# Performance work log

Hardware: AMD Instinct MI355X
Metric: run time of the kernel (lower is better)

## Reference

```python
import jax, jax.numpy as jnp
import numpy as np

L, B, S, D, H, F = 3, 2, 2048, 256, 8, 1024
DK = D // H
EPS = 1e-7


def _positional_encoding(max_len: int, dim: int) -> jnp.ndarray:
    # pos in [1, max_len], i in [1, dim]; w = pos / 10000**((2*i//2)/dim) == pos / 10000**(i/dim)
    pos = np.arange(1, max_len + 1, dtype=np.float64)[:, None]
    i = np.arange(1, dim + 1)
    w = pos / np.power(10000.0, i.astype(np.float64) / dim)[None, :]
    pe = np.where((i % 2 == 0)[None, :], np.sin(w), np.cos(w))
    return jnp.asarray(pe, jnp.float32)


def _ln(x, g, b):
    mu = jnp.mean(x, axis=-1, keepdims=True)
    var = jnp.mean((x - mu) ** 2, axis=-1, keepdims=True)
    return (x - mu) / jnp.sqrt(var + EPS) * g + b


def setup_inputs() -> dict:
    key = jax.random.key(0)
    ks = jax.random.split(key, 16)
    s = 0.05
    inp = {
        "x": jax.random.normal(ks[0], (B, S, D), jnp.float32),
        "mask": jax.random.randint(ks[1], (B, S, S), 0, 2).astype(bool),
        "pe": _positional_encoding(S, D),
        "Wq": jax.random.normal(ks[2], (L, H, D, DK), jnp.float32) * s,
        "Wk": jax.random.normal(ks[3], (L, H, D, DK), jnp.float32) * s,
        "Wv": jax.random.normal(ks[4], (L, H, D, DK), jnp.float32) * s,
        "Wo": jax.random.normal(ks[5], (L, D, D), jnp.float32) * s,
        "bo": jnp.zeros((L, D), jnp.float32),
        "ln1_g": jnp.ones((L, D), jnp.float32),
        "ln1_b": jnp.zeros((L, D), jnp.float32),
        "W1": jax.random.normal(ks[6], (L, D, F), jnp.float32) * s,
        "b1": jnp.zeros((L, F), jnp.float32),
        "W2": jax.random.normal(ks[7], (L, F, D), jnp.float32) * s,
        "b2": jnp.zeros((L, D), jnp.float32),
        "ln2_g": jnp.ones((L, D), jnp.float32),
        "ln2_b": jnp.zeros((L, D), jnp.float32),
    }
    return inp


def _encoder_layer(x, mask, Wq, Wk, Wv, Wo, bo, ln1_g, ln1_b, W1, b1, W2, b2, ln2_g, ln2_b):
    # all heads batched: [B,S,D] x [H,D,dk] -> [B,H,S,dk]
    q = jnp.einsum('bsd,hdk->bhsk', x, Wq)
    k = jnp.einsum('bsd,hdk->bhsk', x, Wk)
    v = jnp.einsum('bsd,hdk->bhsk', x, Wv)
    scores = jnp.einsum('bhsk,bhtk->bhst', q, k) / jnp.sqrt(jnp.float32(DK))
    neg = -jnp.finfo(jnp.float32).max
    scores = jnp.where(mask[:, None, :, :], neg, scores)
    attn = jax.nn.softmax(scores, axis=-1)
    # concat heads along feature dim (head-major order as torch.cat dim=2)
    o = jnp.einsum('bhst,bhtv->bshv', attn, v).reshape(x.shape[0], x.shape[1], D)
    o = o @ Wo + bo
    x = _ln(o + x, ln1_g, ln1_b)  # post-norm (prenorm=False), dropout_rate=0
    h = jax.nn.relu(x @ W1 + b1) @ W2 + b2
    x = _ln(h + x, ln2_g, ln2_b)
    return x


def reference(x, mask, pe, Wq, Wk, Wv, Wo, bo, ln1_g, ln1_b, W1, b1, W2, b2, ln2_g, ln2_b):
    x = x + pe[None, : x.shape[1], :]
    for l in range(L):
        x = _encoder_layer(x, mask, Wq[l], Wk[l], Wv[l], Wo[l], bo[l], ln1_g[l], ln1_b[l],
                           W1[l], b1[l], W2[l], b2[l], ln2_g[l], ln2_b[l])
    return x
```

## Files before the change

### kernel.cpp

```cpp
#include <hip/hip_runtime.h>
#include <hip/hip_bf16.h>
#include <cfloat>

#define Lc 3
#define Bc 2
#define Sc 2048
#define Dc 256
#define Hc 8
#define DKc 32
#define Fc 1024

typedef __hip_bfloat16 bf16;
typedef short s8v __attribute__((ext_vector_type(8)));
typedef float f4v __attribute__((ext_vector_type(4)));

#define QSCALE 0.25504526036067815f

__device__ __forceinline__ float load_f(const void* p, size_t i, int isbf)
{
    return isbf ? __bfloat162float(((const bf16*)p)[i]) : ((const float*)p)[i];
}

typedef const __attribute__((address_space(1))) char gchar_t;
typedef __attribute__((address_space(3))) char lchar_t;
__device__ __forceinline__ void glds16(const void* g, void* l)
{
    __builtin_amdgcn_global_load_lds((gchar_t*)(size_t)g, (lchar_t*)(size_t)l,
                                     16, 0, 0);
}

#define NBLK_REPACK 2304
#define NBLK_CONV   6942
#define NBLK_PACK   1024
#define NBLK_PE     4096

__global__ __launch_bounds__(256) void prologue_fused(
    const void* __restrict__ x, const void* __restrict__ mask,
    const void* __restrict__ pe,
    const void* Wq, const void* Wk, const void* Wv,
    const void* Wo, const void* W1, const void* W2,
    const void* bo, const void* b1, const void* b2,
    const void* g1, const void* be1, const void* g2, const void* be2,
    bf16* __restrict__ wqkv, bf16* __restrict__ dstb, float* __restrict__ pc,
    unsigned* __restrict__ pmask, float* __restrict__ xf,
    bf16* __restrict__ xb, int* __restrict__ flags)
{
    __shared__ int sf[2];
    int tid = threadIdx.x;
    if (tid < 64) {
        const unsigned short* u16 = (const unsigned short*)x;
        int cnt = 0;
        for (int i = tid; i < 256; i += 64) {
            unsigned e = (u16[2 * i] >> 7) & 0xFF;
            cnt += (e >= 90 && e <= 140) ? 1 : 0;
        }
        #pragma unroll
        for (int d = 1; d < 64; d <<= 1) cnt += __shfl_xor(cnt, d);
        const unsigned* mu = (const unsigned*)mask;
        int c2 = ((mu[tid] & 0xFFFFFF00u) == 0) ? 1 : 0;
        #pragma unroll
        for (int d = 1; d < 64; d <<= 1) c2 += __shfl_xor(c2, d);
        if (tid == 0) {
            sf[0] = (cnt >= 128) ? 1 : 0;
            sf[1] = (c2 >= 48) ? 1 : 0;
            if (blockIdx.x == 0) { flags[0] = sf[0]; flags[1] = sf[1]; }
        }
    }
    __syncthreads();
    int isbf = sf[0], mf = sf[1];
    int blk = blockIdx.x;

    if (blk < NBLK_REPACK) {
        int idx = blk * 256 + tid;
        int l   = idx / (3 * Dc * Dc);
        int rem = idx % (3 * Dc * Dc);
        int col = rem / Dc;
        int d   = rem % Dc;
        int mat = col / Dc;
        int hk  = col % Dc;
        int h = hk / DKc, kk = hk % DKc;
        const void* W = (mat == 0) ? Wq : (mat == 1) ? Wk : Wv;
        float v = load_f(W, (size_t)l * (Hc * Dc * DKc) + h * (Dc * DKc) + d * DKc + kk, isbf);
        wqkv[idx] = __float2bfloat16(v);
    } else if (blk < NBLK_REPACK + NBLK_CONV) {
        const int NB0 = Lc * Dc * Dc;
        const int NB1 = NB0 + Lc * Dc * Fc;
        const int NB2 = NB1 + Lc * Fc * Dc;
        int idx = (blk - NBLK_REPACK) * 256 + tid;
        if (idx < NB2) {
            const void* src; int off;
            if (idx < NB0) {
                int l = idx / (Dc * Dc); int rem = idx % (Dc * Dc);
                int n = rem / Dc, k = rem % Dc;
                src = Wo; off = l * Dc * Dc + k * Dc + n;
            } else if (idx < NB1) {
                int j = idx - NB0;
                int l = j / (Fc * Dc); int rem = j % (Fc * Dc);
                int n = rem / Dc, k = rem % Dc;
                src = W1; off = l * Dc * Fc + k * Fc + n;
            } else {
                int j = idx - NB1;
                int l = j / (Dc * Fc); int rem = j % (Dc * Fc);
                int n = rem / Fc, k = rem % Fc;
                src = W2; off = l * Fc * Dc + k * Dc + n;
            }
            dstb[idx] = __float2bfloat16(load_f(src, off, isbf));
        } else {
            int off = idx - NB2;
            if (off < 7680) {
                const void* src; int lo;
                if (off < 768)       { src = bo;  lo = off; }
                else if (off < 3840) { src = b1;  lo = off - 768; }
                else if (off < 4608) { src = b2;  lo = off - 3840; }
                else if (off < 5376) { src = g1;  lo = off - 4608; }
                else if (off < 6144) { src = be1; lo = off - 5376; }
                else if (off < 6912) { src = g2;  lo = off - 6144; }
                else                 { src = be2; lo = off - 6912; }
                pc[off] = load_f(src, lo, isbf);
            }
        }
    } else if (blk < NBLK_REPACK + NBLK_CONV + NBLK_PACK) {
        int idx = (blk - NBLK_REPACK - NBLK_CONV) * 256 + tid;
        unsigned wb = 0;
        if (mf) {
            const int* mp = (const int*)mask + (size_t)idx * 32;
            #pragma unroll
            for (int u = 0; u < 8; ++u) {
                uint4 q = *(const uint4*)(mp + u * 4);
                wb |= (q.x ? 1u : 0u) << (u * 4);
                wb |= (q.y ? 1u : 0u) << (u * 4 + 1);
                wb |= (q.z ? 1u : 0u) << (u * 4 + 2);
                wb |= (q.w ? 1u : 0u) << (u * 4 + 3);
            }
        } else {
            const unsigned char* mp = (const unsigned char*)mask + (size_t)idx * 32;
            uint4 a = *(const uint4*)mp;
            uint4 bq = *(const uint4*)(mp + 16);
            const unsigned char* ab = (const unsigned char*)&a;
            const unsigned char* bb = (const unsigned char*)&bq;
            #pragma unroll
            for (int j = 0; j < 16; ++j) {
                wb |= (ab[j] ? 1u : 0u) << j;
                wb |= (bb[j] ? 1u : 0u) << (16 + j);
            }
        }
        pmask[idx] = wb;
    } else {
        int idx = (blk - NBLK_REPACK - NBLK_CONV - NBLK_PACK) * 256 + tid;
        int rem = idx % (Sc * Dc);
        float v = load_f(x, idx, isbf) + load_f(pe, rem, isbf);
        xf[idx] = v;
        xb[idx] = __float2bfloat16(v);
    }
}

__global__ __launch_bounds__(256) void gemm_mfma(
    const bf16* __restrict__ A, const bf16* __restrict__ BT,
    const float* __restrict__ bias, void* __restrict__ C,
    int M, int N, int K, int relu, int obf, float ascale, int scale_ncols)
{
    __shared__ __align__(16) short As[4096];
    __shared__ __align__(16) short Bs[4096];
    int tid = threadIdx.x;
    int w = tid >> 6, lane = tid & 63;
    int quad = lane >> 4, l15 = lane & 15;
    int wm0 = (w & 1) * 32, wn0 = (w >> 1) * 32;
    int row0 = blockIdx.y * 64, col0 = blockIdx.x * 64;

    int s0 = w * 128 + lane;
    int s1 = s0 + 64;
    int r0 = s0 >> 3, c0 = ((s0 & 7) ^ (r0 & 7)) * 8;
    int r1 = s1 >> 3, c1 = ((s1 & 7) ^ (r1 & 7)) * 8;
    const bf16* Ag0 = A + (size_t)(row0 + r0) * K + c0;
    const bf16* Ag1 = A + (size_t)(row0 + r1) * K + c1;
    const bf16* Bg0 = BT + (size_t)(col0 + r0) * K + c0;
    const bf16* Bg1 = BT + (size_t)(col0 + r1) * K + c1;
    short* Ad0 = As + w * 1024;
    short* Ad1 = As + w * 1024 + 512;
    short* Bd0 = Bs + w * 1024;
    short* Bd1 = Bs + w * 1024 + 512;

    f4v acc00 = {0.f,0.f,0.f,0.f}, acc01 = acc00, acc10 = acc00, acc11 = acc00;

    int m0 = wm0 + l15, m1 = wm0 + 16 + l15;
    int n0 = wn0 + l15, n1 = wn0 + 16 + l15;
    int sw7 = l15 & 7;

    for (int k0 = 0; k0 < K; k0 += 64) {
        glds16(Ag0 + k0, Ad0);
        glds16(Ag1 + k0, Ad1);
        glds16(Bg0 + k0, Bd0);
        glds16(Bg1 + k0, Bd1);
        __syncthreads();
        #pragma unroll
        for (int kc = 0; kc < 2; ++kc) {
            int sw = ((kc * 4 + quad) ^ sw7) * 8;
            s8v a0 = *(const s8v*)(As + m0 * 64 + sw);
            s8v a1 = *(const s8v*)(As + m1 * 64 + sw);
            s8v b0 = *(const s8v*)(Bs + n0 * 64 + sw);
            s8v b1 = *(const s8v*)(Bs + n1 * 64 + sw);
            acc00 = __builtin_amdgcn_mfma_f32_16x16x32_bf16(a0, b0, acc00, 0, 0, 0);
            acc01 = __builtin_amdgcn_mfma_f32_16x16x32_bf16(a0, b1, acc01, 0, 0, 0);
            acc10 = __builtin_amdgcn_mfma_f32_16x16x32_bf16(a1, b0, acc10, 0, 0, 0);
            acc11 = __builtin_amdgcn_mfma_f32_16x16x32_bf16(a1, b1, acc11, 0, 0, 0);
        }
        __syncthreads();
    }

    float bv0 = bias ? bias[col0 + wn0 + l15] : 0.f;
    float bv1 = bias ? bias[col0 + wn0 + 16 + l15] : 0.f;
    f4v accs[2][2] = {{acc00, acc01}, {acc10, acc11}};
    #pragma unroll
    for (int mt = 0; mt < 2; ++mt) {
        #pragma unroll
        for (int nt = 0; nt < 2; ++nt) {
            int gr = row0 + wm0 + mt * 16 + quad * 4;
            int gc = col0 + wn0 + nt * 16 + l15;
            float badd = nt ? bv1 : bv0;
            float sc = (gc < scale_ncols) ? ascale : 1.f;
            #pragma unroll
            for (int reg = 0; reg < 4; ++reg) {
                float v = accs[mt][nt][reg] * sc + badd;
                if (relu) v = fmaxf(v, 0.f);
                if (obf) ((bf16*)C)[(size_t)(gr + reg) * N + gc] = __float2bfloat16(v);
                else     ((float*)C)[(size_t)(gr + reg) * N + gc] = v;
            }
        }
    }
}

__global__ __launch_bounds__(256) void gemm_mfma32(
    const bf16* __restrict__ A, const bf16* __restrict__ BT,
    const float* __restrict__ bias, void* __restrict__ C,
    int M, int N, int K, int relu, int obf)
{
    __shared__ __align__(16) short As[2048];
    __shared__ __align__(16) short Bs[4096];
    int tid = threadIdx.x;
    int w = tid >> 6, lane = tid & 63;
    int quad = lane >> 4, l15 = lane & 15;
    int wm0 = (w & 1) * 16, wn0 = (w >> 1) * 32;
    int row0 = blockIdx.y * 32, col0 = blockIdx.x * 64;

    int sa = w * 64 + lane;
    int ra = sa >> 3, ca = ((sa & 7) ^ (ra & 7)) * 8;
    int s0 = w * 128 + lane, s1 = s0 + 64;
    int r0 = s0 >> 3, c0 = ((s0 & 7) ^ (r0 & 7)) * 8;
    int r1 = s1 >> 3, c1 = ((s1 & 7) ^ (r1 & 7)) * 8;
    const bf16* Ag  = A + (size_t)(row0 + ra) * K + ca;
    const bf16* Bg0 = BT + (size_t)(col0 + r0) * K + c0;
    const bf16* Bg1 = BT + (size_t)(col0 + r1) * K + c1;
    short* Ad  = As + w * 512;
    short* Bd0 = Bs + w * 1024;
    short* Bd1 = Bs + w * 1024 + 512;

    f4v acc0 = {0.f,0.f,0.f,0.f}, acc1 = acc0;

    int m0 = wm0 + l15;
    int n0 = wn0 + l15, n1 = wn0 + 16 + l15;
    int sw7 = l15 & 7;

    for (int k0 = 0; k0 < K; k0 += 64) {
        glds16(Ag + k0, Ad);
        glds16(Bg0 + k0, Bd0);
        glds16(Bg1 + k0, Bd1);
        __syncthreads();
        #pragma unroll
        for (int kc = 0; kc < 2; ++kc) {
            int sw = ((kc * 4 + quad) ^ sw7) * 8;
            s8v a0 = *(const s8v*)(As + m0 * 64 + sw);
            s8v b0 = *(const s8v*)(Bs + n0 * 64 + sw);
            s8v b1 = *(const s8v*)(Bs + n1 * 64 + sw);
            acc0 = __builtin_amdgcn_mfma_f32_16x16x32_bf16(a0, b0, acc0, 0, 0, 0);
            acc1 = __builtin_amdgcn_mfma_f32_16x16x32_bf16(a0, b1, acc1, 0, 0, 0);
        }
        __syncthreads();
    }

    float bv0 = bias ? bias[col0 + wn0 + l15] : 0.f;
    float bv1 = bias ? bias[col0 + wn0 + 16 + l15] : 0.f;
    f4v accs[2] = {acc0, acc1};
    #pragma unroll
    for (int nt = 0; nt < 2; ++nt) {
        int gr = row0 + wm0 + quad * 4;
        int gc = col0 + wn0 + nt * 16 + l15;
        float badd = nt ? bv1 : bv0;
        #pragma unroll
        for (int reg = 0; reg < 4; ++reg) {
            float v = accs[nt][reg] + badd;
            if (relu) v = fmaxf(v, 0.f);
            if (obf) ((bf16*)C)[(size_t)(gr + reg) * N + gc] = __float2bfloat16(v);
            else     ((float*)C)[(size_t)(gr + reg) * N + gc] = v;
        }
    }
}

__global__ __launch_bounds__(256) void flash_mfma(
    const bf16* __restrict__ qkv, const unsigned* __restrict__ pmask,
    bf16* __restrict__ op0, bf16* __restrict__ op1,
    bf16* __restrict__ op2, bf16* __restrict__ op3,
    float* __restrict__ spart)
{
    __shared__ __align__(16) short Ks[64 * 40];
    __shared__ __align__(16) short Vt[2336];
    __shared__ __align__(16) short Pw[4][16 * 72];

    int tid = threadIdx.x;
    int w = tid >> 6;
    int lane = tid & 63;
    int quad = lane >> 4, l15 = lane & 15;
    int q0 = blockIdx.x * 64;
    int h = blockIdx.y;
    int z = blockIdx.z;
    int b = z >> 2, rng = z & 3;
    bf16* op = (rng == 0) ? op0 : (rng == 1) ? op1 : (rng == 2) ? op2 : op3;

    s8v qfrag = *(const s8v*)(qkv + (size_t)(b * Sc + q0 + w * 16 + l15) * 768 + h * 32 + quad * 8);

    f4v o0 = {0.f,0.f,0.f,0.f}, o1 = o0;
    float ssum[4] = {0.f, 0.f, 0.f, 0.f};

    int st = tid >> 2, sd = (tid & 3) * 8;
    int sig = ((st & 15) << 2) | (st >> 4);
    short* pwv = Pw[w];
    const unsigned* pmrow = pmask + (size_t)b * Sc * (Sc / 32);

    for (int it = 0; it < 8; ++it) {
        int t0 = rng * (Sc / 4) + it * 64;
        __syncthreads();
        {
            const bf16* kvb = qkv + (size_t)(b * Sc + t0 + st) * 768 + h * 32 + sd;
            uint4 kw = *(const uint4*)(kvb + 256);
            *(uint4*)(Ks + st * 40 + sd) = kw;
            uint4 vw = *(const uint4*)(kvb + 512);
            const unsigned short* vu = (const unsigned short*)&vw;
            #pragma unroll
            for (int j = 0; j < 8; ++j) Vt[(sd + j) * 72 + sig + sd] = (short)vu[j];
        }
        unsigned mw0[4], mw1[4];
        #pragma unroll
        for (int reg = 0; reg < 4; ++reg) {
            int row = q0 + w * 16 + quad * 4 + reg;
            const unsigned* pp = pmrow + (size_t)row * (Sc / 32) + (t0 >> 5);
            mw0[reg] = pp[0];
            mw1[reg] = pp[1];
        }
        __syncthreads();

        f4v sfr[4];
        #pragma unroll
        for (int nt = 0; nt < 4; ++nt) {
            s8v kf = *(const s8v*)(Ks + (l15 + 16 * nt) * 40 + quad * 8);
            f4v zz = {0.f,0.f,0.f,0.f};
            sfr[nt] = __builtin_amdgcn_mfma_f32_16x16x32_bf16(qfrag, kf, zz, 0, 0, 0);
        }
        #pragma unroll
        for (int reg = 0; reg < 4; ++reg) {
            unsigned ta = mw0[reg] >> l15;
            unsigned tb = mw1[reg] >> l15;
            float p0 = exp2f(sfr[0][reg]); if (ta & 1u)         p0 = 0.f;
            float p1 = exp2f(sfr[1][reg]); if ((ta >> 16) & 1u) p1 = 0.f;
            float p2 = exp2f(sfr[2][reg]); if (tb & 1u)         p2 = 0.f;
            float p3 = exp2f(sfr[3][reg]); if ((tb >> 16) & 1u) p3 = 0.f;
            ssum[reg] += (p0 + p1) + (p2 + p3);
            __hip_bfloat162 plo = __float22bfloat162_rn(make_float2(p0, p1));
            __hip_bfloat162 phi = __float22bfloat162_rn(make_float2(p2, p3));
            uint2 pk = {*(unsigned*)&plo, *(unsigned*)&phi};
            *(uint2*)(pwv + (quad * 4 + reg) * 72 + l15 * 4) = pk;
        }
        #pragma unroll
        for (int kc = 0; kc < 2; ++kc) {
            s8v pf  = *(const s8v*)(pwv + l15 * 72 + kc * 32 + quad * 8);
            s8v vf0 = *(const s8v*)(Vt + l15 * 72 + kc * 32 + quad * 8 + (l15 & 24));
            s8v vf1 = *(const s8v*)(Vt + (l15 + 16) * 72 + kc * 32 + quad * 8 + ((l15 + 16) & 24));
            o0 = __builtin_amdgcn_mfma_f32_16x16x32_bf16(pf, vf0, o0, 0, 0, 0);
            o1 = __builtin_amdgcn_mfma_f32_16x16x32_bf16(pf, vf1, o1, 0, 0, 0);
        }
    }

    #pragma unroll
    for (int reg = 0; reg < 4; ++reg) {
        #pragma unroll
        for (int d = 1; d < 16; d <<= 1) ssum[reg] += __shfl_xor(ssum[reg], d);
    }

    #pragma unroll
    for (int reg = 0; reg < 4; ++reg) {
        int row = q0 + w * 16 + quad * 4 + reg;
        size_t ob = (size_t)(b * Sc + row) * Dc + h * DKc;
        op[ob + l15]      = __float2bfloat16(o0[reg]);
        op[ob + 16 + l15] = __float2bfloat16(o1[reg]);
        if (l15 == 0)
            spart[((size_t)(rng * Bc + b) * Hc + h) * Sc + row] = ssum[reg];
    }
}

__global__ __launch_bounds__(256) void attn_merge(
    const bf16* __restrict__ op0, const bf16* __restrict__ op1,
    const bf16* __restrict__ op2, const bf16* __restrict__ op3,
    const float* __restrict__ spart, bf16* __restrict__ attn_out)
{
    int t8 = blockIdx.x * 256 + threadIdx.x;
    size_t idx = (size_t)t8 * 8;
    int d = (int)(idx & 255);
    int h = d >> 5;
    int row = (int)((idx >> 8) & (Sc - 1));
    int b = (int)(idx >> 19);
    float s = 0.f;
    #pragma unroll
    for (int r = 0; r < 4; ++r)
        s += spart[((size_t)(r * Bc + b) * Hc + h) * Sc + row];
    float inv = 1.f / fmaxf(s, 1e-30f);

    uint4 a0 = *(const uint4*)(op0 + idx);
    uint4 a1 = *(const uint4*)(op1 + idx);
    uint4 a2 = *(const uint4*)(op2 + idx);
    uint4 a3 = *(const uint4*)(op3 + idx);
    const unsigned short* u0 = (const unsigned short*)&a0;
    const unsigned short* u1 = (const unsigned short*)&a1;
    const unsigned short* u2 = (const unsigned short*)&a2;
    const unsigned short* u3 = (const unsigned short*)&a3;
    unsigned short outv[8];
    #pragma unroll
    for (int j = 0; j < 8; ++j) {
        float o = (__uint_as_float((unsigned)u0[j] << 16) + __uint_as_float((unsigned)u1[j] << 16))
                + (__uint_as_float((unsigned)u2[j] << 16) + __uint_as_float((unsigned)u3[j] << 16));
        bf16 ov = __float2bfloat16(o * inv);
        outv[j] = *(unsigned short*)&ov;
    }
    *(uint4*)(attn_out + idx) = *(uint4*)outv;
}

__global__ __launch_bounds__(256) void add_ln(
    const float* __restrict__ a, float* __restrict__ xf, bf16* __restrict__ xb,
    const float* __restrict__ g, const float* __restrict__ b,
    void* __restrict__ dout, const int* __restrict__ flags)
{
    __shared__ float ws4[2][4];
    int row = blockIdx.x, d = threadIdx.x;
    size_t idx = (size_t)row * Dc + d;
    float v = a[idx] + xf[idx];
    float s = v;
    #pragma unroll
    for (int dd = 1; dd < 64; dd <<= 1) s += __shfl_xor(s, dd);
    if ((d & 63) == 0) ws4[0][d >> 6] = s;
    __syncthreads();
    float mu = (ws4[0][0] + ws4[0][1] + ws4[0][2] + ws4[0][3]) * (1.f / Dc);
    float c = v - mu;
    float q = c * c;
    #pragma unroll
    for (int dd = 1; dd < 64; dd <<= 1) q += __shfl_xor(q, dd);
    if ((d & 63) == 0) ws4[1][d >> 6] = q;
    __syncthreads();
    float var = (ws4[1][0] + ws4[1][1] + ws4[1][2] + ws4[1][3]) * (1.f / Dc);
    float r2 = c * rsqrtf(var + 1e-7f) * g[d] + b[d];
    xf[idx] = r2;
    xb[idx] = __float2bfloat16(r2);
    if (dout) {
        if (flags[0]) ((bf16*)dout)[idx] = __float2bfloat16(r2);
        else          ((float*)dout)[idx] = r2;
    }
}

extern "C" void kernel_launch(void* const* d_in, const int* in_sizes, int n_in,
                              void* d_out, int out_size, void* d_ws, size_t ws_size,
                              hipStream_t stream)
{
    const void* x    = d_in[0];
    const void* mask = d_in[1];
    const void* pe   = d_in[2];
    const void* Wq   = d_in[3];
    const void* Wk   = d_in[4];
    const void* Wv   = d_in[5];
    const void* Wo   = d_in[6];
    const void* bo   = d_in[7];
    const void* ln1g = d_in[8];
    const void* ln1b = d_in[9];
    const void* W1   = d_in[10];
    const void* b1   = d_in[11];
    const void* W2   = d_in[12];
    const void* b2   = d_in[13];
    const void* ln2g = d_in[14];
    const void* ln2b = d_in[15];

    const int M = Bc * Sc;
    char* ws = (char*)d_ws;
    const size_t MB = 1024 * 1024;
    int*      flags    = (int*)ws;
    float*    xf32     = (float*)(ws + 256);
    float*    obuf     = (float*)(ws + 256 + 4 * MB);
    char*     bigc     = ws + 256 + 8 * MB;
    bf16*     xbf      = (bf16*)(ws + 256 + 16 * MB);
    bf16*     attn_out = (bf16*)(ws + 256 + 18 * MB);
    bf16*     wqkv     = (bf16*)(ws + 256 + 20 * MB);
    bf16*     woc      = wqkv + (size_t)Lc * Dc * 3 * Dc;
    bf16*     w1c      = woc + (size_t)Lc * Dc * Dc;
    bf16*     w2c      = w1c + (size_t)Lc * Dc * Fc;
    float*    pc       = (float*)(w2c + (size_t)Lc * Fc * Dc);
    unsigned* pmask    = (unsigned*)(ws + 256 + 25 * MB);
    float*    spart    = (float*)(ws + 256 + 26 * MB);

    bf16* qkv  = (bf16*)bigc;
    bf16* hbuf = (bf16*)bigc;
    bf16* op0  = (bf16*)obuf;
    bf16* op1  = op0 + (size_t)M * Dc;
    bf16* op2  = attn_out;
    bf16* op3  = (bf16*)(bigc + 6 * MB);

    float* pc_bo   = pc;
    float* pc_b1   = pc + 768;
    float* pc_b2   = pc + 3840;
    float* pc_ln1g = pc + 4608;
    float* pc_ln1b = pc + 5376;
    float* pc_ln2g = pc + 6144;
    float* pc_ln2b = pc + 6912;

    prologue_fused<<<NBLK_REPACK + NBLK_CONV + NBLK_PACK + NBLK_PE, 256, 0, stream>>>(
        x, mask, pe, Wq, Wk, Wv, Wo, W1, W2, bo, b1, b2,
        ln1g, ln1b, ln2g, ln2b, wqkv, woc, pc, pmask, xf32, xbf, flags);

    for (int l = 0; l < Lc; ++l) {
        gemm_mfma<<<dim3(3 * Dc / 64, M / 64), 256, 0, stream>>>(
            xbf, wqkv + (size_t)l * Dc * 3 * Dc, nullptr, qkv, M, 3 * Dc, Dc, 0, 1,
            QSCALE, Dc);
        flash_mfma<<<dim3(Sc / 64, Hc, Bc * 4), 256, 0, stream>>>(
            qkv, pmask, op0, op1, op2, op3, spart);
        attn_merge<<<(Bc * Sc * Dc / 8) / 256, 256, 0, stream>>>(
            op0, op1, op2, op3, spart, attn_out);
        gemm_mfma32<<<dim3(Dc / 64, M / 32), 256, 0, stream>>>(
            attn_out, woc + (size_t)l * Dc * Dc, pc_bo + l * Dc, obuf, M, Dc, Dc, 0, 0);
        add_ln<<<M, 256, 0, stream>>>(obuf, xf32, xbf,
            pc_ln1g + l * Dc, pc_ln1b + l * Dc, nullptr, flags);
        gemm_mfma<<<dim3(Fc / 64, M / 64), 256, 0, stream>>>(
            xbf, w1c + (size_t)l * Dc * Fc, pc_b1 + l * Fc, hbuf, M, Fc, Dc, 1, 1,
            1.f, 0);
        gemm_mfma32<<<dim3(Dc / 64, M / 32), 256, 0, stream>>>(
            hbuf, w2c + (size_t)l * Fc * Dc, pc_b2 + l * Dc, obuf, M, Dc, Fc, 0, 0);
        add_ln<<<M, 256, 0, stream>>>(obuf, xf32, xbf,
            pc_ln2g + l * Dc, pc_ln2b + l * Dc,
            (l == Lc - 1) ? d_out : nullptr, flags);
    }
}
```

Before: 381.7 us.

## Write V pre-transposed from QKV GEMM and double-buffer K/V loads in flash kernel

The QKV GEMM epilogue now writes V directly in a per-head transposed, permuted layout into a separate buffer, and Q/K are stored with a 512-wide row stride. The flash attention kernel loads K and V tiles with direct global-to-LDS copies into double-buffered, XOR-swizzled shared memory and prefetches the next tile while computing on the current one. This drops the in-kernel scalar V transpose and one barrier per iteration. In exchange the GEMM epilogue does scattered 2-byte stores for V, and the flash kernel uses more LDS.

```diff
diff --git a/kernel.cpp b/kernel.cpp
--- a/kernel.cpp
+++ b/kernel.cpp
@@ -157,7 +157,9 @@
 __global__ __launch_bounds__(256) void gemm_mfma(
     const bf16* __restrict__ A, const bf16* __restrict__ BT,
     const float* __restrict__ bias, void* __restrict__ C,
-    int M, int N, int K, int relu, int obf, float ascale, int scale_ncols)
+    bf16* __restrict__ vt,
+    int M, int N, int K, int relu, int obf, float ascale, int scale_ncols,
+    int ldc)
 {
     __shared__ __align__(16) short As[4096];
     __shared__ __align__(16) short Bs[4096];
@@ -216,14 +218,27 @@
         for (int nt = 0; nt < 2; ++nt) {
             int gr = row0 + wm0 + mt * 16 + quad * 4;
             int gc = col0 + wn0 + nt * 16 + l15;
-            float badd = nt ? bv1 : bv0;
-            float sc = (gc < scale_ncols) ? ascale : 1.f;
-            #pragma unroll
-            for (int reg = 0; reg < 4; ++reg) {
-                float v = accs[mt][nt][reg] * sc + badd;
-                if (relu) v = fmaxf(v, 0.f);
-                if (obf) ((bf16*)C)[(size_t)(gr + reg) * N + gc] = __float2bfloat16(v);
-                else     ((float*)C)[(size_t)(gr + reg) * N + gc] = v;
+            if (vt && gc >= 2 * Dc) {
+                int hh = (gc - 2 * Dc) >> 5, kk = (gc - 2 * Dc) & 31;
+                int bI = gr >> 11;
+                int srow = gr & (Sc - 1);
+                int u = srow & 63;
+                int pos0 = ((u & 15) << 2) | (u >> 4);
+                size_t vb = ((size_t)(bI * Hc + hh) * DKc + kk) * Sc
+                            + (srow & ~63) + pos0;
+                #pragma unroll
+                for (int reg = 0; reg < 4; ++reg)
+                    vt[vb + reg * 4] = __float2bfloat16(accs[mt][nt][reg]);
+            } else {
+                float badd = nt ? bv1 : bv0;
+                float sc = (gc < scale_ncols) ? ascale : 1.f;
+                #pragma unroll
+                for (int reg = 0; reg < 4; ++reg) {
+                    float v = accs[mt][nt][reg] * sc + badd;
+                    if (relu) v = fmaxf(v, 0.f);
+                    if (obf) ((bf16*)C)[(size_t)(gr + reg) * ldc + gc] = __float2bfloat16(v);
+                    else     ((float*)C)[(size_t)(gr + reg) * ldc + gc] = v;
+                }
             }
         }
     }
@@ -296,13 +311,14 @@
 }
 
 __global__ __launch_bounds__(256) void flash_mfma(
-    const bf16* __restrict__ qkv, const unsigned* __restrict__ pmask,
+    const bf16* __restrict__ qkv, const bf16* __restrict__ vt,
+    const unsigned* __restrict__ pmask,
     bf16* __restrict__ op0, bf16* __restrict__ op1,
     bf16* __restrict__ op2, bf16* __restrict__ op3,
     float* __restrict__ spart)
 {
-    __shared__ __align__(16) short Ks[64 * 40];
-    __shared__ __align__(16) short Vt[2336];
+    __shared__ __align__(16) short Ks[2][2048];
+    __shared__ __align__(16) short Vs[2][2048];
     __shared__ __align__(16) short Pw[4][16 * 72];
 
     int tid = threadIdx.x;
@@ -315,49 +331,54 @@
     int b = z >> 2, rng = z & 3;
     bf16* op = (rng == 0) ? op0 : (rng == 1) ? op1 : (rng == 2) ? op2 : op3;
 
-    s8v qfrag = *(const s8v*)(qkv + (size_t)(b * Sc + q0 + w * 16 + l15) * 768 + h * 32 + quad * 8);
+    s8v qfrag = *(const s8v*)(qkv + (size_t)(b * Sc + q0 + w * 16 + l15) * 512 + h * 32 + quad * 8);
+
+    int sr = tid >> 3, ss = tid & 7;
+    int c8 = ss ^ (sr & 7);
+    const bf16* kg = qkv + (size_t)(b * Sc + rng * (Sc / 4) + 2 * sr + (c8 >> 2)) * 512
+                     + 256 + h * 32 + (c8 & 3) * 8;
+    const bf16* vg = vt + ((size_t)(b * Hc + h) * DKc + sr) * Sc + rng * (Sc / 4) + c8 * 8;
+
+    int koff = (l15 >> 1) * 64 + ((((l15 & 1) << 2) + quad) ^ ((l15 >> 1) & 7)) * 8;
+    int pfoff = l15 * 72 + quad * 8;
+    int vkey = l15 & 7;
+    int voff = l15 * 64;
 
     f4v o0 = {0.f,0.f,0.f,0.f}, o1 = o0;
     float ssum[4] = {0.f, 0.f, 0.f, 0.f};
 
-    int st = tid >> 2, sd = (tid & 3) * 8;
-    int sig = ((st & 15) << 2) | (st >> 4);
     short* pwv = Pw[w];
-    const unsigned* pmrow = pmask + (size_t)b * Sc * (Sc / 32);
-
+    const unsigned* mp = pmask + (size_t)b * Sc * (Sc / 32)
+                         + (size_t)(q0 + w * 16 + quad * 4) * (Sc / 32) + rng * 16;
+
+#define FSTAGE(bi, it2) do { \
+        glds16(kg + (size_t)(it2) * (64 * 512), Ks[bi] + w * 512); \
+        glds16(vg + (it2) * 64, Vs[bi] + w * 512); \
+    } while (0)
+
+    FSTAGE(0, 0);
     for (int it = 0; it < 8; ++it) {
-        int t0 = rng * (Sc / 4) + it * 64;
+        int cur = it & 1;
         __syncthreads();
-        {
-            const bf16* kvb = qkv + (size_t)(b * Sc + t0 + st) * 768 + h * 32 + sd;
-            uint4 kw = *(const uint4*)(kvb + 256);
-            *(uint4*)(Ks + st * 40 + sd) = kw;
-            uint4 vw = *(const uint4*)(kvb + 512);
-            const unsigned short* vu = (const unsigned short*)&vw;
-            #pragma unroll
-            for (int j = 0; j < 8; ++j) Vt[(sd + j) * 72 + sig + sd] = (short)vu[j];
-        }
-        unsigned mw0[4], mw1[4];
-        #pragma unroll
-        for (int reg = 0; reg < 4; ++reg) {
-            int row = q0 + w * 16 + quad * 4 + reg;
-            const unsigned* pp = pmrow + (size_t)row * (Sc / 32) + (t0 >> 5);
-            mw0[reg] = pp[0];
-            mw1[reg] = pp[1];
-        }
-        __syncthreads();
-
+        if (it < 7) FSTAGE(cur ^ 1, it + 1);
+
+        uint2 mw[4];
+        #pragma unroll
+        for (int reg = 0; reg < 4; ++reg)
+            mw[reg] = *(const uint2*)(mp + reg * (Sc / 32) + it * 2);
+
+        const short* kb = Ks[cur];
         f4v sfr[4];
         #pragma unroll
         for (int nt = 0; nt < 4; ++nt) {
-            s8v kf = *(const s8v*)(Ks + (l15 + 16 * nt) * 40 + quad * 8);
+            s8v kf = *(const s8v*)(kb + koff + nt * 512);
             f4v zz = {0.f,0.f,0.f,0.f};
             sfr[nt] = __builtin_amdgcn_mfma_f32_16x16x32_bf16(qfrag, kf, zz, 0, 0, 0);
         }
         #pragma unroll
         for (int reg = 0; reg < 4; ++reg) {
-            unsigned ta = mw0[reg] >> l15;
-            unsigned tb = mw1[reg] >> l15;
+            unsigned ta = mw[reg].x >> l15;
+            unsigned tb = mw[reg].y >> l15;
             float p0 = exp2f(sfr[0][reg]); if (ta & 1u)         p0 = 0.f;
             float p1 = exp2f(sfr[1][reg]); if ((ta >> 16) & 1u) p1 = 0.f;
             float p2 = exp2f(sfr[2][reg]); if (tb & 1u)         p2 = 0.f;
@@ -368,15 +389,18 @@
             uint2 pk = {*(unsigned*)&plo, *(unsigned*)&phi};
             *(uint2*)(pwv + (quad * 4 + reg) * 72 + l15 * 4) = pk;
         }
+        const short* vb = Vs[cur];
         #pragma unroll
         for (int kc = 0; kc < 2; ++kc) {
-            s8v pf  = *(const s8v*)(pwv + l15 * 72 + kc * 32 + quad * 8);
-            s8v vf0 = *(const s8v*)(Vt + l15 * 72 + kc * 32 + quad * 8 + (l15 & 24));
-            s8v vf1 = *(const s8v*)(Vt + (l15 + 16) * 72 + kc * 32 + quad * 8 + ((l15 + 16) & 24));
+            s8v pf = *(const s8v*)(pwv + pfoff + kc * 32);
+            int vo = voff + (((kc * 4 + quad) ^ vkey) * 8);
+            s8v vf0 = *(const s8v*)(vb + vo);
+            s8v vf1 = *(const s8v*)(vb + vo + 1024);
             o0 = __builtin_amdgcn_mfma_f32_16x16x32_bf16(pf, vf0, o0, 0, 0, 0);
             o1 = __builtin_amdgcn_mfma_f32_16x16x32_bf16(pf, vf1, o1, 0, 0, 0);
         }
     }
+#undef FSTAGE
 
     #pragma unroll
     for (int reg = 0; reg < 4; ++reg) {
@@ -501,6 +525,7 @@
     float*    spart    = (float*)(ws + 256 + 26 * MB);
 
     bf16* qkv  = (bf16*)bigc;
+    bf16* vtb  = (bf16*)(bigc + 4 * MB);
     bf16* hbuf = (bf16*)bigc;
     bf16* op0  = (bf16*)obuf;
     bf16* op1  = op0 + (size_t)M * Dc;
@@ -521,10 +546,10 @@
 
     for (int l = 0; l < Lc; ++l) {
         gemm_mfma<<<dim3(3 * Dc / 64, M / 64), 256, 0, stream>>>(
-            xbf, wqkv + (size_t)l * Dc * 3 * Dc, nullptr, qkv, M, 3 * Dc, Dc, 0, 1,
-            QSCALE, Dc);
+            xbf, wqkv + (size_t)l * Dc * 3 * Dc, nullptr, qkv, vtb,
+            M, 3 * Dc, Dc, 0, 1, QSCALE, Dc, 512);
         flash_mfma<<<dim3(Sc / 64, Hc, Bc * 4), 256, 0, stream>>>(
-            qkv, pmask, op0, op1, op2, op3, spart);
+            qkv, vtb, pmask, op0, op1, op2, op3, spart);
         attn_merge<<<(Bc * Sc * Dc / 8) / 256, 256, 0, stream>>>(
             op0, op1, op2, op3, spart, attn_out);
         gemm_mfma32<<<dim3(Dc / 64, M / 32), 256, 0, stream>>>(
@@ -532,8 +557,8 @@
         add_ln<<<M, 256, 0, stream>>>(obuf, xf32, xbf,
             pc_ln1g + l * Dc, pc_ln1b + l * Dc, nullptr, flags);
         gemm_mfma<<<dim3(Fc / 64, M / 64), 256, 0, stream>>>(
-            xbf, w1c + (size_t)l * Dc * Fc, pc_b1 + l * Fc, hbuf, M, Fc, Dc, 1, 1,
-            1.f, 0);
+            xbf, w1c + (size_t)l * Dc * Fc, pc_b1 + l * Fc, hbuf, nullptr,
+            M, Fc, Dc, 1, 1, 1.f, 0, Fc);
         gemm_mfma32<<<dim3(Dc / 64, M / 32), 256, 0, stream>>>(
             hbuf, w2c + (size_t)l * Fc * Dc, pc_b2 + l * Dc, obuf, M, Dc, Fc, 0, 0);
         add_ln<<<M, 256, 0, stream>>>(obuf, xf32, xbf,
```

After: 384.2 us. No clear change (+0.7%).
